# Kernel optimization log

Hardware: AMD Instinct MI355X
Metric: run time of the kernel (lower is better)

Reference implementation:

```python
import jax, jax.numpy as jnp
import numpy as np

ENT_TYPES = 9
INNER_DIM = 64


def setup_inputs() -> dict:
    key = jax.random.key(0)
    k1, k2 = jax.random.split(key)
    B, S, H = 8, 1024, 768
    last_hidden_state = jax.random.normal(k1, (B, S, H), dtype=jnp.float32)
    attention_mask = jnp.ones((B, S), dtype=jnp.float32)
    dense_w = jax.random.normal(k2, (ENT_TYPES * INNER_DIM * 2, H), dtype=jnp.float32) * (1.0 / np.sqrt(H))
    dense_b = jnp.zeros((ENT_TYPES * INNER_DIM * 2,), dtype=jnp.float32)
    return {
        "last_hidden_state": last_hidden_state,
        "attention_mask": attention_mask,
        "dense_w": dense_w,
        "dense_b": dense_b,
    }


def _sinusoidal_pos_emb(seq_len: int, output_dim: int, dtype):
    # (seq_len, output_dim) interleaved as [sin0, cos0, sin1, cos1, ...]
    position = jnp.arange(seq_len, dtype=dtype)[:, None]              # (S, 1)
    indices = jnp.arange(output_dim // 2, dtype=dtype)
    inv_freq = jnp.power(jnp.asarray(10000.0, dtype), -2.0 * indices / output_dim)
    ang = position * inv_freq                                         # (S, D/2)
    emb = jnp.stack([jnp.sin(ang), jnp.cos(ang)], axis=-1)            # (S, D/2, 2)
    return emb.reshape(seq_len, output_dim)


def reference(last_hidden_state, attention_mask, dense_w, dense_b):
    B, S, H = last_hidden_state.shape
    D = INNER_DIM
    E = ENT_TYPES

    # dense projection then split into per-entity-type q/k of width D each
    out = last_hidden_state @ dense_w.T + dense_b                     # (B, S, 2*E*D)
    out = out.reshape(B, S, E, 2 * D)                                 # (B, S, E, 2D)
    qw, kw = out[..., :D], out[..., D:]                               # (B, S, E, D)

    # RoPE: duplicated cos/sin pairs, half-rotation
    pos = _sinusoidal_pos_emb(S, D, last_hidden_state.dtype)          # (S, D)
    cos_pos = jnp.repeat(pos[:, 1::2], 2, axis=-1)[None, :, None, :]  # (1, S, 1, D)
    sin_pos = jnp.repeat(pos[:, 0::2], 2, axis=-1)[None, :, None, :]

    def rotate_half(x):
        x1, x2 = x[..., : D // 2], x[..., D // 2 :]
        return jnp.concatenate([-x2, x1], axis=-1)

    qw = qw * cos_pos + rotate_half(qw) * sin_pos
    kw = kw * cos_pos + rotate_half(kw) * sin_pos

    # pairwise entity scores
    logits = jnp.einsum("bmhd,bnhd->bhmn", qw, kw) / jnp.sqrt(jnp.asarray(D, logits_dtype := last_hidden_state.dtype))

    # padding mask along key axis (as in original)
    pad_mask = attention_mask[:, None, None, :]                       # (B, 1, 1, S)
    logits = logits * pad_mask - (1.0 - pad_mask) * 10000.0

    # upper-triangular validity mask (start <= end)
    tri = jnp.triu(jnp.ones((S, S), dtype=logits.dtype))[None, None]  # (1, 1, S, S)
    logits = logits - (1.0 - tri) * 10000.0
    return logits
```

## Files before the change

### kernel.cpp

```cpp
#include <hip/hip_runtime.h>

#define BB 8
#define SS 1024
#define HH 768
#define EE 9
#define DD 64
#define NCOL (EE * 2 * DD)

typedef __bf16 bf16x8 __attribute__((ext_vector_type(8)));
typedef float f32x4 __attribute__((ext_vector_type(4)));

__device__ __forceinline__ unsigned short f2b(float f) {
    unsigned int x = __float_as_uint(f);
    unsigned int r = (x + 0x7fffu + ((x >> 16) & 1u)) >> 16;
    return (unsigned short)r;
}

#define LDA1 40
__global__ __launch_bounds__(256) void dense_rope_mfma(
    const float* __restrict__ lhs,
    const float* __restrict__ W,
    const float* __restrict__ bias,
    unsigned short* __restrict__ q_ws,
    unsigned short* __restrict__ k_ws) {
    __shared__ unsigned short As[128 * LDA1];
    __shared__ unsigned short Bs[128 * LDA1];

    const int t = threadIdx.x;
    const int lane = t & 63, wave = t >> 6;
    const int quad = lane >> 4, lr = lane & 15;
    const int wm = wave >> 1, wn = wave & 1;
    const int j0 = blockIdx.x * 128;
    const int m0 = blockIdx.y * 128;

    f32x4 acc[4][4] = {};

    for (int kt = 0; kt < HH / 32; ++kt) {
        const int k0 = kt * 32;
        float4 av[4], bv[4];
#pragma unroll
        for (int i = 0; i < 4; ++i) {
            int idx = t + i * 256;
            int row = idx >> 3, c4 = (idx & 7) * 4;
            av[i] = *(const float4*)&lhs[(size_t)(m0 + row) * HH + k0 + c4];
            bv[i] = *(const float4*)&W[(size_t)(j0 + row) * HH + k0 + c4];
        }
        __syncthreads();
#pragma unroll
        for (int i = 0; i < 4; ++i) {
            int idx = t + i * 256;
            int row = idx >> 3, c4 = (idx & 7) * 4;
            ushort4 a4 = {f2b(av[i].x), f2b(av[i].y), f2b(av[i].z), f2b(av[i].w)};
            ushort4 b4 = {f2b(bv[i].x), f2b(bv[i].y), f2b(bv[i].z), f2b(bv[i].w)};
            *(ushort4*)&As[row * LDA1 + c4] = a4;
            *(ushort4*)&Bs[row * LDA1 + c4] = b4;
        }
        __syncthreads();

        bf16x8 af[4], bf[4];
#pragma unroll
        for (int mt = 0; mt < 4; ++mt)
            af[mt] = *(const bf16x8*)&As[(wm * 64 + mt * 16 + lr) * LDA1 + quad * 8];
#pragma unroll
        for (int nt = 0; nt < 4; ++nt)
            bf[nt] = *(const bf16x8*)&Bs[(wn * 64 + nt * 16 + lr) * LDA1 + quad * 8];
#pragma unroll
        for (int mt = 0; mt < 4; ++mt)
#pragma unroll
            for (int nt = 0; nt < 4; ++nt)
                acc[mt][nt] = __builtin_amdgcn_mfma_f32_16x16x32_bf16(
                    af[mt], bf[nt], acc[mt][nt], 0, 0, 0);
    }

    const int gcol0 = j0 + wn * 64;
    const int g = gcol0 >> 6;
    const int e = g >> 1;
    unsigned short* dst = (g & 1) ? k_ws : q_ws;
    const int b_idx = m0 >> 10;
    const size_t zbase = (size_t)(b_idx * EE + e) * SS;
    const float L2_1E4_D32 = 0.4152410118609203f;

    float bb[4], invf[4];
#pragma unroll
    for (int nt = 0; nt < 4; ++nt) {
        bb[nt] = bias[gcol0 + nt * 16 + lr];
        int half = (nt * 16 + lr) >> 1;
        invf[nt] = exp2f(-(float)half * L2_1E4_D32);
    }
    const int s0 = (m0 & (SS - 1)) + wm * 64;
#pragma unroll
    for (int mt = 0; mt < 4; ++mt) {
#pragma unroll
        for (int reg = 0; reg < 4; ++reg) {
            const int s = s0 + mt * 16 + quad * 4 + reg;
            float c[4];
#pragma unroll
            for (int nt = 0; nt < 4; ++nt) c[nt] = acc[mt][nt][reg] + bb[nt];
#pragma unroll
            for (int nt = 0; nt < 4; ++nt) {
                float rot = (nt < 2) ? -c[nt + 2] : c[nt - 2];
                float ang = (float)s * invf[nt];
                float sv, cv;
                __sincosf(ang, &sv, &cv);
                const int d = nt * 16 + lr;
                dst[(zbase + s) * DD + d] = f2b(c[nt] * cv + rot * sv);
            }
        }
    }
}

#define LDA2 72
__global__ __launch_bounds__(256) void logits_mfma(
    const unsigned short* __restrict__ q_ws,
    const unsigned short* __restrict__ k_ws,
    const float* __restrict__ mask,
    float* __restrict__ out) {
    __shared__ unsigned short Qs[128 * LDA2];
    __shared__ unsigned short Ks[128 * LDA2];

    const int t = threadIdx.x;
    const int lane = t & 63, wave = t >> 6;
    const int quad = lane >> 4, lr = lane & 15;
    const int wm = wave >> 1, wn = wave & 1;
    const int n0 = blockIdx.x * 128;
    const int m0 = blockIdx.y * 128;
    const int z = blockIdx.z;
    const int b_idx = z / EE;

    const uint4* qsrc = (const uint4*)(q_ws + ((size_t)z * SS + m0) * DD);
    const uint4* ksrc = (const uint4*)(k_ws + ((size_t)z * SS + n0) * DD);
#pragma unroll
    for (int i = 0; i < 4; ++i) {
        int idx = t + i * 256;
        int row = idx >> 3, c8 = (idx & 7) * 8;
        uint4 qv = qsrc[idx];
        uint4 kv = ksrc[idx];
        *(uint4*)&Qs[row * LDA2 + c8] = qv;
        *(uint4*)&Ks[row * LDA2 + c8] = kv;
    }
    __syncthreads();

    f32x4 acc[4][4] = {};
#pragma unroll
    for (int ks = 0; ks < DD; ks += 32) {
        bf16x8 af[4], bf[4];
#pragma unroll
        for (int mt = 0; mt < 4; ++mt)
            af[mt] = *(const bf16x8*)&Qs[(wm * 64 + mt * 16 + lr) * LDA2 + ks + quad * 8];
#pragma unroll
        for (int nt = 0; nt < 4; ++nt)
            bf[nt] = *(const bf16x8*)&Ks[(wn * 64 + nt * 16 + lr) * LDA2 + ks + quad * 8];
#pragma unroll
        for (int mt = 0; mt < 4; ++mt)
#pragma unroll
            for (int nt = 0; nt < 4; ++nt)
                acc[mt][nt] = __builtin_amdgcn_mfma_f32_16x16x32_bf16(
                    af[mt], bf[nt], acc[mt][nt], 0, 0, 0);
    }

    float p[4];
#pragma unroll
    for (int nt = 0; nt < 4; ++nt)
        p[nt] = mask[b_idx * SS + n0 + wn * 64 + nt * 16 + lr];

    float* outz = out + (size_t)z * SS * SS;
#pragma unroll
    for (int mt = 0; mt < 4; ++mt) {
#pragma unroll
        for (int reg = 0; reg < 4; ++reg) {
            const int m = m0 + wm * 64 + mt * 16 + quad * 4 + reg;
#pragma unroll
            for (int nt = 0; nt < 4; ++nt) {
                const int n = n0 + wn * 64 + nt * 16 + lr;
                float v = acc[mt][nt][reg] * 0.125f;
                v = v * p[nt] - (1.0f - p[nt]) * 10000.0f;
                if (n < m) v -= 10000.0f;
                outz[(size_t)m * SS + n] = v;
            }
        }
    }
}

extern "C" void kernel_launch(void* const* d_in, const int* in_sizes, int n_in,
                              void* d_out, int out_size, void* d_ws, size_t ws_size,
                              hipStream_t stream) {
    const float* lhs  = (const float*)d_in[0];
    const float* mask = (const float*)d_in[1];
    const float* W    = (const float*)d_in[2];
    const float* bias = (const float*)d_in[3];
    float* out = (float*)d_out;

    unsigned short* q_ws = (unsigned short*)d_ws;
    unsigned short* k_ws = q_ws + (size_t)BB * EE * SS * DD;

    dim3 g1(NCOL / 128, (BB * SS) / 128);
    dense_rope_mfma<<<g1, 256, 0, stream>>>(lhs, W, bias, q_ws, k_ws);

    dim3 g2(SS / 128, SS / 128, BB * EE);
    logits_mfma<<<g2, 256, 0, stream>>>(q_ws, k_ws, mask, out);
}
```

Measured before the change: 399.2 us.

## Pre-convert inputs to bf16 in a separate kernel, deepen K tile, use hardware sin/cos

```diff
diff --git a/kernel.cpp b/kernel.cpp
--- a/kernel.cpp
+++ b/kernel.cpp
@@ -16,15 +16,35 @@
     return (unsigned short)r;
 }
 
-#define LDA1 40
+__global__ __launch_bounds__(256) void convert_bf16(
+    const float* __restrict__ lhs, const float* __restrict__ W,
+    unsigned short* __restrict__ lhs_b, unsigned short* __restrict__ W_b) {
+    const int NL4 = (BB * SS * HH) / 4;
+    const int NW4 = (NCOL * HH) / 4;
+    int i = blockIdx.x * blockDim.x + threadIdx.x;
+    if (i < NL4) {
+        float4 v = ((const float4*)lhs)[i];
+        ushort4 u = {f2b(v.x), f2b(v.y), f2b(v.z), f2b(v.w)};
+        ((ushort4*)lhs_b)[i] = u;
+    } else {
+        int j = i - NL4;
+        if (j < NW4) {
+            float4 v = ((const float4*)W)[j];
+            ushort4 u = {f2b(v.x), f2b(v.y), f2b(v.z), f2b(v.w)};
+            ((ushort4*)W_b)[j] = u;
+        }
+    }
+}
+
+#define LDK 72
 __global__ __launch_bounds__(256) void dense_rope_mfma(
-    const float* __restrict__ lhs,
-    const float* __restrict__ W,
+    const unsigned short* __restrict__ A,
+    const unsigned short* __restrict__ Wb,
     const float* __restrict__ bias,
     unsigned short* __restrict__ q_ws,
     unsigned short* __restrict__ k_ws) {
-    __shared__ unsigned short As[128 * LDA1];
-    __shared__ unsigned short Bs[128 * LDA1];
+    __shared__ unsigned short As[128 * LDK];
+    __shared__ unsigned short Bs[128 * LDK];
 
     const int t = threadIdx.x;
     const int lane = t & 63, wave = t >> 6;
@@ -35,41 +55,42 @@
 
     f32x4 acc[4][4] = {};
 
-    for (int kt = 0; kt < HH / 32; ++kt) {
-        const int k0 = kt * 32;
-        float4 av[4], bv[4];
+    for (int kt = 0; kt < HH / 64; ++kt) {
+        const int k0 = kt * 64;
+        uint4 av[4], bv[4];
 #pragma unroll
         for (int i = 0; i < 4; ++i) {
             int idx = t + i * 256;
-            int row = idx >> 3, c4 = (idx & 7) * 4;
-            av[i] = *(const float4*)&lhs[(size_t)(m0 + row) * HH + k0 + c4];
-            bv[i] = *(const float4*)&W[(size_t)(j0 + row) * HH + k0 + c4];
+            int row = idx >> 3, c8 = (idx & 7) * 8;
+            av[i] = *(const uint4*)&A[(size_t)(m0 + row) * HH + k0 + c8];
+            bv[i] = *(const uint4*)&Wb[(size_t)(j0 + row) * HH + k0 + c8];
         }
         __syncthreads();
 #pragma unroll
         for (int i = 0; i < 4; ++i) {
             int idx = t + i * 256;
-            int row = idx >> 3, c4 = (idx & 7) * 4;
-            ushort4 a4 = {f2b(av[i].x), f2b(av[i].y), f2b(av[i].z), f2b(av[i].w)};
-            ushort4 b4 = {f2b(bv[i].x), f2b(bv[i].y), f2b(bv[i].z), f2b(bv[i].w)};
-            *(ushort4*)&As[row * LDA1 + c4] = a4;
-            *(ushort4*)&Bs[row * LDA1 + c4] = b4;
+            int row = idx >> 3, c8 = (idx & 7) * 8;
+            *(uint4*)&As[row * LDK + c8] = av[i];
+            *(uint4*)&Bs[row * LDK + c8] = bv[i];
         }
         __syncthreads();
 
-        bf16x8 af[4], bf[4];
-#pragma unroll
-        for (int mt = 0; mt < 4; ++mt)
-            af[mt] = *(const bf16x8*)&As[(wm * 64 + mt * 16 + lr) * LDA1 + quad * 8];
-#pragma unroll
-        for (int nt = 0; nt < 4; ++nt)
-            bf[nt] = *(const bf16x8*)&Bs[(wn * 64 + nt * 16 + lr) * LDA1 + quad * 8];
-#pragma unroll
-        for (int mt = 0; mt < 4; ++mt)
+#pragma unroll
+        for (int kh = 0; kh < 2; ++kh) {
+            bf16x8 af[4], bf[4];
+#pragma unroll
+            for (int mt = 0; mt < 4; ++mt)
+                af[mt] = *(const bf16x8*)&As[(wm * 64 + mt * 16 + lr) * LDK + kh * 32 + quad * 8];
 #pragma unroll
             for (int nt = 0; nt < 4; ++nt)
-                acc[mt][nt] = __builtin_amdgcn_mfma_f32_16x16x32_bf16(
-                    af[mt], bf[nt], acc[mt][nt], 0, 0, 0);
+                bf[nt] = *(const bf16x8*)&Bs[(wn * 64 + nt * 16 + lr) * LDK + kh * 32 + quad * 8];
+#pragma unroll
+            for (int mt = 0; mt < 4; ++mt)
+#pragma unroll
+                for (int nt = 0; nt < 4; ++nt)
+                    acc[mt][nt] = __builtin_amdgcn_mfma_f32_16x16x32_bf16(
+                        af[mt], bf[nt], acc[mt][nt], 0, 0, 0);
+        }
     }
 
     const int gcol0 = j0 + wn * 64;
@@ -79,13 +100,14 @@
     const int b_idx = m0 >> 10;
     const size_t zbase = (size_t)(b_idx * EE + e) * SS;
     const float L2_1E4_D32 = 0.4152410118609203f;
-
-    float bb[4], invf[4];
+    const float INV_2PI = 0.15915494309189535f;
+
+    float bb[4], invrev[4];
 #pragma unroll
     for (int nt = 0; nt < 4; ++nt) {
         bb[nt] = bias[gcol0 + nt * 16 + lr];
         int half = (nt * 16 + lr) >> 1;
-        invf[nt] = exp2f(-(float)half * L2_1E4_D32);
+        invrev[nt] = exp2f(-(float)half * L2_1E4_D32) * INV_2PI;
     }
     const int s0 = (m0 & (SS - 1)) + wm * 64;
 #pragma unroll
@@ -99,9 +121,10 @@
 #pragma unroll
             for (int nt = 0; nt < 4; ++nt) {
                 float rot = (nt < 2) ? -c[nt + 2] : c[nt - 2];
-                float ang = (float)s * invf[nt];
-                float sv, cv;
-                __sincosf(ang, &sv, &cv);
+                float rev = (float)s * invrev[nt];
+                rev -= floorf(rev);
+                float sv = __builtin_amdgcn_sinf(rev);
+                float cv = __builtin_amdgcn_cosf(rev);
                 const int d = nt * 16 + lr;
                 dst[(zbase + s) * DD + d] = f2b(c[nt] * cv + rot * sv);
             }
@@ -190,11 +213,17 @@
     const float* bias = (const float*)d_in[3];
     float* out = (float*)d_out;
 
-    unsigned short* q_ws = (unsigned short*)d_ws;
-    unsigned short* k_ws = q_ws + (size_t)BB * EE * SS * DD;
+    unsigned short* q_ws  = (unsigned short*)d_ws;
+    unsigned short* k_ws  = q_ws + (size_t)BB * EE * SS * DD;
+    unsigned short* lhs_b = k_ws + (size_t)BB * EE * SS * DD;
+    unsigned short* W_b   = lhs_b + (size_t)BB * SS * HH;
+
+    const int NL4 = (BB * SS * HH) / 4;
+    const int NW4 = (NCOL * HH) / 4;
+    convert_bf16<<<(NL4 + NW4 + 255) / 256, 256, 0, stream>>>(lhs, W, lhs_b, W_b);
 
     dim3 g1(NCOL / 128, (BB * SS) / 128);
-    dense_rope_mfma<<<g1, 256, 0, stream>>>(lhs, W, bias, q_ws, k_ws);
+    dense_rope_mfma<<<g1, 256, 0, stream>>>(lhs_b, W_b, bias, q_ws, k_ws);
 
     dim3 g2(SS / 128, SS / 128, BB * EE);
     logits_mfma<<<g2, 256, 0, stream>>>(q_ws, k_ws, mask, out);
```

Result: slower. 430.3 us (+7.8%).
